# Kernel optimization log

Hardware: AMD Instinct MI355X
Metric: run time of the kernel (lower is better)

## Reference

```python
import jax, jax.numpy as jnp
from jax import lax
import numpy as np

TAO = 12   # lag stride
M = 7      # number of lags (m)


def setup_inputs() -> dict:
    key = jax.random.key(0)
    k1, k2, k3, k4, k5 = jax.random.split(key, 5)
    B, L, C, D = 32, 4096, 21, 512
    K = D // C            # kernels per channel = 24
    LO = D - C * K        # leftout channels = 8
    return {
        "x": jax.random.normal(k1, (B, L, C), jnp.float32),
        "conv_w": jax.random.normal(k2, (K, M + 1, 3), jnp.float32) * 0.2,
        "conv_b": jax.random.normal(k3, (K,), jnp.float32) * 0.02,
        "leftout_w": jax.random.normal(k4, (LO, M + 1, 3), jnp.float32) * 0.2,
        "leftout_b": jax.random.normal(k5, (LO,), jnp.float32) * 0.02,
    }


def _circ_conv(x_ncl, w_oik, b_o):
    # circular padding=1, kernel_size=3, stride 1 -> same length
    xp = jnp.pad(x_ncl, ((0, 0), (0, 0), (1, 1)), mode="wrap")
    y = lax.conv_general_dilated(xp, w_oik, (1,), "VALID",
                                 dimension_numbers=("NCW", "OIW", "NCW"))
    return y + b_o[None, :, None]


def reference(x, conv_w, conv_b, leftout_w, leftout_b):
    B, L, C = x.shape
    K = conv_w.shape[0]
    nv = L - M * TAO
    # lagged gather: ext[b, t, c, j] = x[b, m*tao + t - j*tao, c]
    t_idx = jnp.arange(M * TAO, L)                      # [nv]
    offs = jnp.arange(M + 1) * TAO                      # [m+1]
    idx = t_idx[:, None] - offs[None, :]                # [nv, m+1]
    ext = x[:, idx, :]                                  # [B, nv, m+1, C]
    ext = jnp.transpose(ext, (0, 1, 3, 2))              # [B, nv, C, m+1] (channel-major)
    # pad=True: zero-pad the first m*tao timesteps
    ext = jnp.pad(ext, ((0, 0), (M * TAO, 0), (0, 0), (0, 0)))  # [B, L, C, m+1]
    # per-channel chunks as a single batched conv: [B*C, m+1, L]
    xc = jnp.transpose(ext, (0, 2, 3, 1)).reshape(B * C, M + 1, L)
    y = _circ_conv(xc, conv_w, conv_b).reshape(B, C * K, L)      # [B, C*K, L]
    # leftout conv applied to the last channel's chunk only
    last = jnp.transpose(ext[:, :, C - 1, :], (0, 2, 1))         # [B, m+1, L]
    yl = _circ_conv(last, leftout_w, leftout_b)                  # [B, LO, L]
    out = jnp.concatenate([y, yl], axis=1)                       # [B, d_model, L]
    return jnp.transpose(out, (0, 2, 1))                         # [B, L, d_model]
```

## Files before the change

kernel.cpp:

```cpp
#include <hip/hip_runtime.h>

#define LL 4096
#define CC 21
#define TT 64
#define NTB 2
#define XSTR 156
#define STG_N (150 * CC)
#define NSTG 13

typedef float v2f __attribute__((ext_vector_type(2)));
typedef float v4f __attribute__((ext_vector_type(4)));

__device__ __forceinline__ v2f fma2(v2f a, v2f b, v2f c) {
    return __builtin_elementwise_fma(a, b, c);
}

#define RAW_BARRIER() do {                                  \
    asm volatile("s_waitcnt lgkmcnt(0)" ::: "memory");      \
    __builtin_amdgcn_s_barrier();                           \
} while (0)

__device__ __forceinline__ void prefetch_tile(const float* __restrict__ xb,
                                              int baset, int tid, float* pf) {
    const int lo21 = (0 - baset) * CC;
    const int hi21 = (LL - baset) * CC;
    #pragma unroll
    for (int i = 0; i < NSTG; ++i) {
        int e = tid + 256 * i;
        if (e < STG_N) {
            int ofs = baset * CC + e;
            if (e < lo21)  ofs += LL * CC;
            if (e >= hi21) ofs -= LL * CC;
            pf[i] = xb[ofs];
        }
    }
}

__device__ __forceinline__ void write_tile(float* __restrict__ xsb, int tid,
                                           const float* pf) {
    #pragma unroll
    for (int i = 0; i < NSTG; ++i) {
        int e = tid + 256 * i;
        if (e < STG_N) {
            int s = e / CC, c2 = e - s * CC;
            xsb[c2 * XSTR + s] = pf[i];
        }
    }
}

template<bool EDGE>
__device__ __forceinline__ void compute_item(
    const float* __restrict__ xrow, const float* __restrict__ wtc,
    const float* __restrict__ biasc, float* __restrict__ outp,
    int vo0, int d0, int tg, int t0)
{
    v2f acc[16][2];
    {
        v2f b0 = { biasc[vo0],     biasc[vo0 + 1] };
        v2f b1 = { biasc[vo0 + 2], biasc[vo0 + 3] };
        #pragma unroll
        for (int ti = 0; ti < 16; ++ti) { acc[ti][0] = b0; acc[ti][1] = b1; }
    }

    const int base = tg * 16 + 84;

    #pragma unroll 1
    for (int j = 0; j < 8; ++j) {
        const float* wp = &wtc[96 * j + vo0];
        v4f w0 = *reinterpret_cast<const v4f*>(wp);
        v4f w1 = *reinterpret_cast<const v4f*>(wp + 32);
        v4f w2 = *reinterpret_cast<const v4f*>(wp + 64);

        const float* vp = xrow + (base - 12 * j);
        v4f va = *reinterpret_cast<const v4f*>(vp);
        v4f vb = *reinterpret_cast<const v4f*>(vp + 4);
        v4f vc = *reinterpret_cast<const v4f*>(vp + 8);
        v4f vd = *reinterpret_cast<const v4f*>(vp + 12);
        v2f ve = *reinterpret_cast<const v2f*>(vp + 16);
        float v[18] = { va.x, va.y, va.z, va.w, vb.x, vb.y, vb.z, vb.w,
                        vc.x, vc.y, vc.z, vc.w, vd.x, vd.y, vd.z, vd.w,
                        ve.x, ve.y };
        if (EDGE) {
            #pragma unroll
            for (int s = 0; s < 18; ++s)
                if (((t0 + tg * 16 + s - 1) & (LL - 1)) < 84) v[s] = 0.0f;
        }

        #pragma unroll
        for (int ti = 0; ti < 16; ++ti) {
            v2f vv, w;
            vv.x = vv.y = v[ti];
            w.x = w0.x; w.y = w0.y; acc[ti][0] = fma2(vv, w, acc[ti][0]);
            w.x = w0.z; w.y = w0.w; acc[ti][1] = fma2(vv, w, acc[ti][1]);
            vv.x = vv.y = v[ti + 1];
            w.x = w1.x; w.y = w1.y; acc[ti][0] = fma2(vv, w, acc[ti][0]);
            w.x = w1.z; w.y = w1.w; acc[ti][1] = fma2(vv, w, acc[ti][1]);
            vv.x = vv.y = v[ti + 2];
            w.x = w2.x; w.y = w2.y; acc[ti][0] = fma2(vv, w, acc[ti][0]);
            w.x = w2.z; w.y = w2.w; acc[ti][1] = fma2(vv, w, acc[ti][1]);
        }
    }

    #pragma unroll
    for (int ti = 0; ti < 16; ++ti) {
        v4f r = { acc[ti][0].x, acc[ti][0].y, acc[ti][1].x, acc[ti][1].y };
        float* p = outp + (size_t)(tg * 16 + ti) * 512 + d0;
        *reinterpret_cast<v4f*>(p) = r;
    }
}

__global__ __launch_bounds__(256)
__attribute__((amdgpu_waves_per_eu(4, 4)))
void delay_fir_kernel(
    const float* __restrict__ x,
    const float* __restrict__ conv_w,
    const float* __restrict__ conv_b,
    const float* __restrict__ lw,
    const float* __restrict__ lb,
    float* __restrict__ out)
{
    __shared__ __align__(16) float xs[2][CC * XSTR];
    __shared__ __align__(16) float wtc[24 * 32];
    __shared__ float biasc[32];

    const int tid   = threadIdx.x;
    const int b     = blockIdx.y;
    const int tbase = blockIdx.x * (TT * NTB);

    for (int e = tid; e < 24 * 32; e += 256) {
        int jk = e >> 5, vo = e & 31;
        wtc[e] = (vo < 24) ? conv_w[vo * 24 + jk] : lw[(vo - 24) * 24 + jk];
    }
    if (tid < 32) biasc[tid] = (tid < 24) ? conv_b[tid] : lb[tid - 24];

    const float* xb = x + (size_t)b * (LL * CC);

    {
        float pf0[NSTG], pf1[NSTG];
        prefetch_tile(xb, tbase - 85, tid, pf0);
        prefetch_tile(xb, tbase + TT - 85, tid, pf1);
        write_tile(xs[0], tid, pf0);
        write_tile(xs[1], tid, pf1);
    }
    RAW_BARRIER();

    const int l  = tid & 63;
    const int w  = tid >> 6;
    const int d0 = 256 * (w & 1) + 4 * l;
    int c, vo0;
    if (d0 >= 504) { c = 20; vo0 = 24 + (d0 - 504); }
    else           { c = d0 / 24; vo0 = d0 - c * 24; }

    #pragma unroll 1
    for (int tix = 0; tix < NTB; ++tix) {
        const int t0 = tbase + tix * TT;
        const float* xrow = &xs[tix][c * XSTR];
        float* outp = out + ((size_t)b * LL + t0) * 512;
        const bool edge = (t0 == 0) | (t0 == TT) | (t0 == LL - TT);
        #pragma unroll 1
        for (int it = 0; it < 2; ++it) {
            int tg = it * 2 + (w >> 1);
            if (edge) compute_item<true >(xrow, wtc, biasc, outp, vo0, d0, tg, t0);
            else      compute_item<false>(xrow, wtc, biasc, outp, vo0, d0, tg, t0);
        }
    }
}

extern "C" void kernel_launch(void* const* d_in, const int* in_sizes, int n_in,
                              void* d_out, int out_size, void* d_ws, size_t ws_size,
                              hipStream_t stream) {
    const float* x      = (const float*)d_in[0];
    const float* conv_w = (const float*)d_in[1];
    const float* conv_b = (const float*)d_in[2];
    const float* lw     = (const float*)d_in[3];
    const float* lb     = (const float*)d_in[4];
    float* out = (float*)d_out;

    dim3 grid(LL / (TT * NTB), 32);
    delay_fir_kernel<<<grid, 256, 0, stream>>>(x, conv_w, conv_b, lw, lb, out);
}
```

Measured before the change: 57.14 us.

## Overlap second tile load with first tile compute and halve accumulator tiles

The kernel now stages only the first input tile into shared memory before computing. The global loads for the second tile are issued early and held in registers while the first tile is computed, then written to shared memory behind a second barrier. Each compute item is split into two 8-timestep halves instead of one 16-timestep pass, which lowers accumulator register pressure at the cost of reloading weights and overlapping input values for each half. The risks are the extra barrier, longer register live ranges from holding the prefetch across the compute, and more redundant shared-memory reads.

```diff
diff --git a/kernel.cpp b/kernel.cpp
--- a/kernel.cpp
+++ b/kernel.cpp
@@ -3,7 +3,6 @@
 #define LL 4096
 #define CC 21
 #define TT 64
-#define NTB 2
 #define XSTR 156
 #define STG_N (150 * CC)
 #define NSTG 13
@@ -49,20 +48,20 @@
 }
 
 template<bool EDGE>
-__device__ __forceinline__ void compute_item(
+__device__ __forceinline__ void compute_half(
     const float* __restrict__ xrow, const float* __restrict__ wtc,
     const float* __restrict__ biasc, float* __restrict__ outp,
-    int vo0, int d0, int tg, int t0)
+    int vo0, int d0, int tg, int ho, int t0)
 {
-    v2f acc[16][2];
+    v2f acc[8][2];
     {
         v2f b0 = { biasc[vo0],     biasc[vo0 + 1] };
         v2f b1 = { biasc[vo0 + 2], biasc[vo0 + 3] };
         #pragma unroll
-        for (int ti = 0; ti < 16; ++ti) { acc[ti][0] = b0; acc[ti][1] = b1; }
-    }
-
-    const int base = tg * 16 + 84;
+        for (int ti = 0; ti < 8; ++ti) { acc[ti][0] = b0; acc[ti][1] = b1; }
+    }
+
+    const int base = tg * 16 + ho + 84;
 
     #pragma unroll 1
     for (int j = 0; j < 8; ++j) {
@@ -74,20 +73,16 @@
         const float* vp = xrow + (base - 12 * j);
         v4f va = *reinterpret_cast<const v4f*>(vp);
         v4f vb = *reinterpret_cast<const v4f*>(vp + 4);
-        v4f vc = *reinterpret_cast<const v4f*>(vp + 8);
-        v4f vd = *reinterpret_cast<const v4f*>(vp + 12);
-        v2f ve = *reinterpret_cast<const v2f*>(vp + 16);
-        float v[18] = { va.x, va.y, va.z, va.w, vb.x, vb.y, vb.z, vb.w,
-                        vc.x, vc.y, vc.z, vc.w, vd.x, vd.y, vd.z, vd.w,
-                        ve.x, ve.y };
+        v2f vc = *reinterpret_cast<const v2f*>(vp + 8);
+        float v[10] = { va.x, va.y, va.z, va.w, vb.x, vb.y, vb.z, vb.w, vc.x, vc.y };
         if (EDGE) {
             #pragma unroll
-            for (int s = 0; s < 18; ++s)
-                if (((t0 + tg * 16 + s - 1) & (LL - 1)) < 84) v[s] = 0.0f;
+            for (int s = 0; s < 10; ++s)
+                if (((t0 + tg * 16 + ho + s - 1) & (LL - 1)) < 84) v[s] = 0.0f;
         }
 
         #pragma unroll
-        for (int ti = 0; ti < 16; ++ti) {
+        for (int ti = 0; ti < 8; ++ti) {
             v2f vv, w;
             vv.x = vv.y = v[ti];
             w.x = w0.x; w.y = w0.y; acc[ti][0] = fma2(vv, w, acc[ti][0]);
@@ -102,10 +97,24 @@
     }
 
     #pragma unroll
-    for (int ti = 0; ti < 16; ++ti) {
+    for (int ti = 0; ti < 8; ++ti) {
         v4f r = { acc[ti][0].x, acc[ti][0].y, acc[ti][1].x, acc[ti][1].y };
-        float* p = outp + (size_t)(tg * 16 + ti) * 512 + d0;
+        float* p = outp + (size_t)(tg * 16 + ho + ti) * 512 + d0;
         *reinterpret_cast<v4f*>(p) = r;
+    }
+}
+
+template<bool EDGE>
+__device__ __forceinline__ void compute_tile(
+    const float* __restrict__ xrow, const float* __restrict__ wtc,
+    const float* __restrict__ biasc, float* __restrict__ outp,
+    int vo0, int d0, int tpair, int t0)
+{
+    #pragma unroll 1
+    for (int it = 0; it < 2; ++it) {
+        int tg = it * 2 + tpair;
+        compute_half<EDGE>(xrow, wtc, biasc, outp, vo0, d0, tg, 0, t0);
+        compute_half<EDGE>(xrow, wtc, biasc, outp, vo0, d0, tg, 8, t0);
     }
 }
 
@@ -125,7 +134,12 @@
 
     const int tid   = threadIdx.x;
     const int b     = blockIdx.y;
-    const int tbase = blockIdx.x * (TT * NTB);
+    const int tbase = blockIdx.x * (TT * 2);
+
+    const float* xb = x + (size_t)b * (LL * CC);
+
+    float pf[NSTG];
+    prefetch_tile(xb, tbase - 85, tid, pf);
 
     for (int e = tid; e < 24 * 32; e += 256) {
         int jk = e >> 5, vo = e & 31;
@@ -133,36 +147,41 @@
     }
     if (tid < 32) biasc[tid] = (tid < 24) ? conv_b[tid] : lb[tid - 24];
 
-    const float* xb = x + (size_t)b * (LL * CC);
-
-    {
-        float pf0[NSTG], pf1[NSTG];
-        prefetch_tile(xb, tbase - 85, tid, pf0);
-        prefetch_tile(xb, tbase + TT - 85, tid, pf1);
-        write_tile(xs[0], tid, pf0);
-        write_tile(xs[1], tid, pf1);
-    }
+    write_tile(xs[0], tid, pf);
+
+    prefetch_tile(xb, tbase + TT - 85, tid, pf);
+
     RAW_BARRIER();
 
     const int l  = tid & 63;
     const int w  = tid >> 6;
     const int d0 = 256 * (w & 1) + 4 * l;
+    const int tpair = w >> 1;
     int c, vo0;
     if (d0 >= 504) { c = 20; vo0 = 24 + (d0 - 504); }
     else           { c = d0 / 24; vo0 = d0 - c * 24; }
 
-    #pragma unroll 1
-    for (int tix = 0; tix < NTB; ++tix) {
-        const int t0 = tbase + tix * TT;
-        const float* xrow = &xs[tix][c * XSTR];
+    {
+        const int t0 = tbase;
+        const float* xrow = &xs[0][c * XSTR];
         float* outp = out + ((size_t)b * LL + t0) * 512;
-        const bool edge = (t0 == 0) | (t0 == TT) | (t0 == LL - TT);
-        #pragma unroll 1
-        for (int it = 0; it < 2; ++it) {
-            int tg = it * 2 + (w >> 1);
-            if (edge) compute_item<true >(xrow, wtc, biasc, outp, vo0, d0, tg, t0);
-            else      compute_item<false>(xrow, wtc, biasc, outp, vo0, d0, tg, t0);
-        }
+        if ((t0 == 0) | (t0 == LL - TT))
+            compute_tile<true >(xrow, wtc, biasc, outp, vo0, d0, tpair, t0);
+        else
+            compute_tile<false>(xrow, wtc, biasc, outp, vo0, d0, tpair, t0);
+    }
+
+    write_tile(xs[1], tid, pf);
+    RAW_BARRIER();
+
+    {
+        const int t0 = tbase + TT;
+        const float* xrow = &xs[1][c * XSTR];
+        float* outp = out + ((size_t)b * LL + t0) * 512;
+        if ((t0 == TT) | (t0 == LL - TT))
+            compute_tile<true >(xrow, wtc, biasc, outp, vo0, d0, tpair, t0);
+        else
+            compute_tile<false>(xrow, wtc, biasc, outp, vo0, d0, tpair, t0);
     }
 }
 
@@ -176,6 +195,6 @@
     const float* lb     = (const float*)d_in[4];
     float* out = (float*)d_out;
 
-    dim3 grid(LL / (TT * NTB), 32);
+    dim3 grid(LL / (TT * 2), 32);
     delay_fir_kernel<<<grid, 256, 0, stream>>>(x, conv_w, conv_b, lw, lb, out);
 }
```

Result: slower. 58.41 us (+2.2%).

## Use a single 128-step shared tile and reuse overlapping lag values in registers

Applied to the files above, without the earlier changes.

The two 64-step shared tiles per block become one 128-step tile with a 214-slot halo, so the two tiles no longer stage overlapping halos separately. In the inner lag loop, values are reused across lags: lag j's 18-value window overlaps lag j-1's by 6 elements, so only 12 new values are loaded from LDS per lag on non-edge tiles. The first lag is peeled out and the FMA block is factored into a helper. Costs: a larger per-thread prefetch register array (18 vs 2x13), and edge handling that now depends on the tile boundaries matching 84.

```diff
diff --git a/kernel.cpp b/kernel.cpp
--- a/kernel.cpp
+++ b/kernel.cpp
@@ -2,11 +2,11 @@
 
 #define LL 4096
 #define CC 21
-#define TT 64
-#define NTB 2
-#define XSTR 156
-#define STG_N (150 * CC)
-#define NSTG 13
+#define TT 128
+#define XSTR 220
+#define STG_SLOTS (TT + 86)
+#define STG_N (STG_SLOTS * CC)
+#define NSTG 18
 
 typedef float v2f __attribute__((ext_vector_type(2)));
 typedef float v4f __attribute__((ext_vector_type(4)));
@@ -45,6 +45,24 @@
             int s = e / CC, c2 = e - s * CC;
             xsb[c2 * XSTR + s] = pf[i];
         }
+    }
+}
+
+__device__ __forceinline__ void fma_block(const float* __restrict__ v,
+                                          v4f w0, v4f w1, v4f w2,
+                                          v2f acc[16][2]) {
+    #pragma unroll
+    for (int ti = 0; ti < 16; ++ti) {
+        v2f vv, w;
+        vv.x = vv.y = v[ti];
+        w.x = w0.x; w.y = w0.y; acc[ti][0] = fma2(vv, w, acc[ti][0]);
+        w.x = w0.z; w.y = w0.w; acc[ti][1] = fma2(vv, w, acc[ti][1]);
+        vv.x = vv.y = v[ti + 1];
+        w.x = w1.x; w.y = w1.y; acc[ti][0] = fma2(vv, w, acc[ti][0]);
+        w.x = w1.z; w.y = w1.w; acc[ti][1] = fma2(vv, w, acc[ti][1]);
+        vv.x = vv.y = v[ti + 2];
+        w.x = w2.x; w.y = w2.y; acc[ti][0] = fma2(vv, w, acc[ti][0]);
+        w.x = w2.z; w.y = w2.w; acc[ti][1] = fma2(vv, w, acc[ti][1]);
     }
 }
 
@@ -63,42 +81,62 @@
     }
 
     const int base = tg * 16 + 84;
-
-    #pragma unroll 1
-    for (int j = 0; j < 8; ++j) {
-        const float* wp = &wtc[96 * j + vo0];
-        v4f w0 = *reinterpret_cast<const v4f*>(wp);
-        v4f w1 = *reinterpret_cast<const v4f*>(wp + 32);
-        v4f w2 = *reinterpret_cast<const v4f*>(wp + 64);
-
-        const float* vp = xrow + (base - 12 * j);
+    float v[18];
+
+    {
+        const float* vp = xrow + base;
         v4f va = *reinterpret_cast<const v4f*>(vp);
         v4f vb = *reinterpret_cast<const v4f*>(vp + 4);
         v4f vc = *reinterpret_cast<const v4f*>(vp + 8);
         v4f vd = *reinterpret_cast<const v4f*>(vp + 12);
         v2f ve = *reinterpret_cast<const v2f*>(vp + 16);
-        float v[18] = { va.x, va.y, va.z, va.w, vb.x, vb.y, vb.z, vb.w,
-                        vc.x, vc.y, vc.z, vc.w, vd.x, vd.y, vd.z, vd.w,
-                        ve.x, ve.y };
+        v[0]=va.x; v[1]=va.y; v[2]=va.z; v[3]=va.w;
+        v[4]=vb.x; v[5]=vb.y; v[6]=vb.z; v[7]=vb.w;
+        v[8]=vc.x; v[9]=vc.y; v[10]=vc.z; v[11]=vc.w;
+        v[12]=vd.x; v[13]=vd.y; v[14]=vd.z; v[15]=vd.w;
+        v[16]=ve.x; v[17]=ve.y;
         if (EDGE) {
             #pragma unroll
             for (int s = 0; s < 18; ++s)
                 if (((t0 + tg * 16 + s - 1) & (LL - 1)) < 84) v[s] = 0.0f;
         }
-
-        #pragma unroll
-        for (int ti = 0; ti < 16; ++ti) {
-            v2f vv, w;
-            vv.x = vv.y = v[ti];
-            w.x = w0.x; w.y = w0.y; acc[ti][0] = fma2(vv, w, acc[ti][0]);
-            w.x = w0.z; w.y = w0.w; acc[ti][1] = fma2(vv, w, acc[ti][1]);
-            vv.x = vv.y = v[ti + 1];
-            w.x = w1.x; w.y = w1.y; acc[ti][0] = fma2(vv, w, acc[ti][0]);
-            w.x = w1.z; w.y = w1.w; acc[ti][1] = fma2(vv, w, acc[ti][1]);
-            vv.x = vv.y = v[ti + 2];
-            w.x = w2.x; w.y = w2.y; acc[ti][0] = fma2(vv, w, acc[ti][0]);
-            w.x = w2.z; w.y = w2.w; acc[ti][1] = fma2(vv, w, acc[ti][1]);
-        }
+        const float* wp = &wtc[vo0];
+        fma_block(v, *reinterpret_cast<const v4f*>(wp),
+                     *reinterpret_cast<const v4f*>(wp + 32),
+                     *reinterpret_cast<const v4f*>(wp + 64), acc);
+    }
+
+    #pragma unroll 1
+    for (int j = 1; j < 8; ++j) {
+        const float* vp = xrow + (base - 12 * j);
+        if (EDGE) {
+            v4f va = *reinterpret_cast<const v4f*>(vp);
+            v4f vb = *reinterpret_cast<const v4f*>(vp + 4);
+            v4f vc = *reinterpret_cast<const v4f*>(vp + 8);
+            v4f vd = *reinterpret_cast<const v4f*>(vp + 12);
+            v2f ve = *reinterpret_cast<const v2f*>(vp + 16);
+            v[0]=va.x; v[1]=va.y; v[2]=va.z; v[3]=va.w;
+            v[4]=vb.x; v[5]=vb.y; v[6]=vb.z; v[7]=vb.w;
+            v[8]=vc.x; v[9]=vc.y; v[10]=vc.z; v[11]=vc.w;
+            v[12]=vd.x; v[13]=vd.y; v[14]=vd.z; v[15]=vd.w;
+            v[16]=ve.x; v[17]=ve.y;
+            #pragma unroll
+            for (int s = 0; s < 18; ++s)
+                if (((t0 + tg * 16 + s - 1) & (LL - 1)) < 84) v[s] = 0.0f;
+        } else {
+            float s0 = v[0], s1 = v[1], s2 = v[2], s3 = v[3], s4 = v[4], s5 = v[5];
+            v4f va = *reinterpret_cast<const v4f*>(vp);
+            v4f vb = *reinterpret_cast<const v4f*>(vp + 4);
+            v4f vc = *reinterpret_cast<const v4f*>(vp + 8);
+            v[0]=va.x; v[1]=va.y; v[2]=va.z; v[3]=va.w;
+            v[4]=vb.x; v[5]=vb.y; v[6]=vb.z; v[7]=vb.w;
+            v[8]=vc.x; v[9]=vc.y; v[10]=vc.z; v[11]=vc.w;
+            v[12]=s0; v[13]=s1; v[14]=s2; v[15]=s3; v[16]=s4; v[17]=s5;
+        }
+        const float* wp = &wtc[96 * j + vo0];
+        fma_block(v, *reinterpret_cast<const v4f*>(wp),
+                     *reinterpret_cast<const v4f*>(wp + 32),
+                     *reinterpret_cast<const v4f*>(wp + 64), acc);
     }
 
     #pragma unroll
@@ -119,13 +157,13 @@
     const float* __restrict__ lb,
     float* __restrict__ out)
 {
-    __shared__ __align__(16) float xs[2][CC * XSTR];
+    __shared__ __align__(16) float xs[CC * XSTR];
     __shared__ __align__(16) float wtc[24 * 32];
     __shared__ float biasc[32];
 
     const int tid   = threadIdx.x;
     const int b     = blockIdx.y;
-    const int tbase = blockIdx.x * (TT * NTB);
+    const int tbase = blockIdx.x * TT;
 
     for (int e = tid; e < 24 * 32; e += 256) {
         int jk = e >> 5, vo = e & 31;
@@ -136,33 +174,29 @@
     const float* xb = x + (size_t)b * (LL * CC);
 
     {
-        float pf0[NSTG], pf1[NSTG];
-        prefetch_tile(xb, tbase - 85, tid, pf0);
-        prefetch_tile(xb, tbase + TT - 85, tid, pf1);
-        write_tile(xs[0], tid, pf0);
-        write_tile(xs[1], tid, pf1);
+        float pf[NSTG];
+        prefetch_tile(xb, tbase - 85, tid, pf);
+        write_tile(xs, tid, pf);
     }
     RAW_BARRIER();
 
     const int l  = tid & 63;
     const int w  = tid >> 6;
     const int d0 = 256 * (w & 1) + 4 * l;
+    const int tpair = w >> 1;
     int c, vo0;
     if (d0 >= 504) { c = 20; vo0 = 24 + (d0 - 504); }
     else           { c = d0 / 24; vo0 = d0 - c * 24; }
 
+    const float* xrow = &xs[c * XSTR];
+    float* outp = out + ((size_t)b * LL + tbase) * 512;
+    const bool edge = (tbase == 0) | (tbase == LL - TT);
+
     #pragma unroll 1
-    for (int tix = 0; tix < NTB; ++tix) {
-        const int t0 = tbase + tix * TT;
-        const float* xrow = &xs[tix][c * XSTR];
-        float* outp = out + ((size_t)b * LL + t0) * 512;
-        const bool edge = (t0 == 0) | (t0 == TT) | (t0 == LL - TT);
-        #pragma unroll 1
-        for (int it = 0; it < 2; ++it) {
-            int tg = it * 2 + (w >> 1);
-            if (edge) compute_item<true >(xrow, wtc, biasc, outp, vo0, d0, tg, t0);
-            else      compute_item<false>(xrow, wtc, biasc, outp, vo0, d0, tg, t0);
-        }
+    for (int it = 0; it < 4; ++it) {
+        int tg = it * 2 + tpair;
+        if (edge) compute_item<true >(xrow, wtc, biasc, outp, vo0, d0, tg, tbase);
+        else      compute_item<false>(xrow, wtc, biasc, outp, vo0, d0, tg, tbase);
     }
 }
 
@@ -176,6 +210,6 @@
     const float* lb     = (const float*)d_in[4];
     float* out = (float*)d_out;
 
-    dim3 grid(LL / (TT * NTB), 32);
+    dim3 grid(LL / TT, 32);
     delay_fir_kernel<<<grid, 256, 0, stream>>>(x, conv_w, conv_b, lw, lb, out);
 }
```

Result: no change. 56.16 us (median of 2 runs) (-1.7%).
